# Performance work log

Hardware: AMD Instinct MI355X
Metric: run time of the kernel (lower is better)

Reference implementation:

```python
import jax, jax.numpy as jnp
import numpy as np


def _conv(x, kernel):
    # x: [N, C, H, W], kernel: [O, I, kh, kw]; torch conv2d padding=1 (symmetric both dims)
    return jax.lax.conv_general_dilated(
        x, kernel, window_strides=(1, 1), padding=((1, 1), (1, 1)),
        dimension_numbers=("NCHW", "OIHW", "NCHW"))


def setup_inputs() -> dict:
    key = jax.random.key(0)
    k1, k2 = jax.random.split(key)
    shape = (2, 7, 7, 3, 256, 256)  # bs, ah, aw, c, h, w
    infer = jax.random.normal(k1, shape, dtype=jnp.float32)
    ref = jax.random.normal(k2, shape, dtype=jnp.float32)
    return {"infer": infer, "ref": ref}


def reference(infer, ref):
    bs, ah, aw, c, h, w = infer.shape
    x = infer.reshape(bs * ah * aw, c, h, w)
    y = ref.reshape(bs * ah * aw, c, h, w)
    # fixed gradient kernels, identical across all 3x3 in/out channel pairs
    kh = jnp.broadcast_to(
        jnp.array([-0.5, 0.0, 0.5], jnp.float32).reshape(1, 1, 1, 3), (3, 3, 1, 3))
    kv = jnp.broadcast_to(
        jnp.array([-0.5, 0.0, 0.5], jnp.float32).reshape(1, 1, 3, 1), (3, 3, 3, 1))
    # torch padding=1 on a (1,3) kernel -> output (h+2, w); on (3,1) -> (h, w+2)
    loss_h = jnp.mean(jnp.abs(_conv(x, kh) - _conv(y, kh)))
    loss_v = jnp.mean(jnp.abs(_conv(x, kv) - _conv(y, kv)))
    return (loss_h + loss_v) / 2.0
```

## Files before the change

### kernel.cpp

```cpp
#include <hip/hip_runtime.h>


#define W 256
#define NIMG 98
#define CH_STRIDE 65536
#define TH 4
#define NSTRIP 64
#define NBLK (NIMG * NSTRIP)
#define SCALE (0.25f / 6472704.0f)

__device__ __forceinline__ float4 load_D_row(const float* __restrict__ xb,
                                             const float* __restrict__ yb, int r) {
  float4 d = make_float4(0.f, 0.f, 0.f, 0.f);
  if (r >= 0 && r < 256) {
    const int off = r * W;
    #pragma unroll
    for (int c = 0; c < 3; ++c) {
      float4 xv = *(const float4*)(xb + c * CH_STRIDE + off);
      float4 yv = *(const float4*)(yb + c * CH_STRIDE + off);
      d.x += xv.x - yv.x;
      d.y += xv.y - yv.y;
      d.z += xv.z - yv.z;
      d.w += xv.w - yv.w;
    }
  }
  return d;
}

__global__ __launch_bounds__(64) void detail_stage1(
    const float* __restrict__ x, const float* __restrict__ y,
    float* __restrict__ partial) {
  const int lane  = threadIdx.x;
  const int b     = blockIdx.x;
  const int n     = b >> 6;
  const int strip = b & 63;
  const int r0    = strip * TH;

  const float* xb = x + (size_t)n * 3 * CH_STRIDE + (lane << 2);
  const float* yb = y + (size_t)n * 3 * CH_STRIDE + (lane << 2);

  float4 Dm = load_D_row(xb, yb, r0 - 1);
  float4 D0 = load_D_row(xb, yb, r0);
  float acc = 0.f;

  #pragma unroll
  for (int i = 0; i < TH; ++i) {
    float4 Dp = load_D_row(xb, yb, r0 + i + 1);
    float left  = __shfl_up(D0.w, 1, 64);
    float right = __shfl_down(D0.x, 1, 64);
    if (lane == 0)  left  = 0.f;
    if (lane == 63) right = 0.f;
    acc += fabsf(D0.y - left)  + fabsf(D0.z - D0.x)
         + fabsf(D0.w - D0.y)  + fabsf(right - D0.z)
         + fabsf(Dp.x - Dm.x)  + fabsf(Dp.y - Dm.y)
         + fabsf(Dp.z - Dm.z)  + fabsf(Dp.w - Dm.w);
    Dm = D0; D0 = Dp;
  }

  #pragma unroll
  for (int off = 32; off > 0; off >>= 1)
    acc += __shfl_down(acc, off, 64);
  if (lane == 0) partial[b] = acc;
}

__global__ __launch_bounds__(64) void detail_stage1_atomic(
    const float* __restrict__ x, const float* __restrict__ y,
    float* __restrict__ out) {
  const int lane  = threadIdx.x;
  const int b     = blockIdx.x;
  const int n     = b >> 6;
  const int strip = b & 63;
  const int r0    = strip * TH;
  const float* xb = x + (size_t)n * 3 * CH_STRIDE + (lane << 2);
  const float* yb = y + (size_t)n * 3 * CH_STRIDE + (lane << 2);
  float4 Dm = load_D_row(xb, yb, r0 - 1);
  float4 D0 = load_D_row(xb, yb, r0);
  float acc = 0.f;
  #pragma unroll
  for (int i = 0; i < TH; ++i) {
    float4 Dp = load_D_row(xb, yb, r0 + i + 1);
    float left  = __shfl_up(D0.w, 1, 64);
    float right = __shfl_down(D0.x, 1, 64);
    if (lane == 0)  left  = 0.f;
    if (lane == 63) right = 0.f;
    acc += fabsf(D0.y - left)  + fabsf(D0.z - D0.x)
         + fabsf(D0.w - D0.y)  + fabsf(right - D0.z)
         + fabsf(Dp.x - Dm.x)  + fabsf(Dp.y - Dm.y)
         + fabsf(Dp.z - Dm.z)  + fabsf(Dp.w - Dm.w);
    Dm = D0; D0 = Dp;
  }
  #pragma unroll
  for (int off = 32; off > 0; off >>= 1)
    acc += __shfl_down(acc, off, 64);
  if (lane == 0) atomicAdd(out, acc * SCALE);
}

__global__ __launch_bounds__(256) void detail_stage2(
    const float* __restrict__ partial, float* __restrict__ out) {
  float acc = 0.f;
  for (int i = threadIdx.x; i < NBLK; i += 256) acc += partial[i];
  #pragma unroll
  for (int off = 32; off > 0; off >>= 1)
    acc += __shfl_down(acc, off, 64);
  __shared__ float ws[4];
  if ((threadIdx.x & 63) == 0) ws[threadIdx.x >> 6] = acc;
  __syncthreads();
  if (threadIdx.x == 0) out[0] = (ws[0] + ws[1] + ws[2] + ws[3]) * SCALE;
}

extern "C" void kernel_launch(void* const* d_in, const int* in_sizes, int n_in,
                              void* d_out, int out_size, void* d_ws, size_t ws_size,
                              hipStream_t stream) {
  const float* infer = (const float*)d_in[0];
  const float* ref   = (const float*)d_in[1];
  float* out = (float*)d_out;

  if (ws_size >= NBLK * sizeof(float)) {
    float* partial = (float*)d_ws;
    detail_stage1<<<NBLK, 64, 0, stream>>>(infer, ref, partial);
    detail_stage2<<<1, 256, 0, stream>>>(partial, out);
  } else {
    hipMemsetAsync(out, 0, sizeof(float), stream);
    detail_stage1_atomic<<<NBLK, 64, 0, stream>>>(infer, ref, out);
  }
}
```

Measured before the change: 173.5 us.

## Stage channel-summed difference rows in shared memory with 256-thread blocks

Each block now covers 8 output rows with 256 threads. Four wavefronts cooperatively load the 10 halo rows, each issuing all its loads up front, and write the channel-summed difference into a shared-memory tile. Each thread then computes the horizontal and vertical gradient terms for one column from shared memory. This lowers halo overhead from 6/4 to 10/8 rows loaded per output row and exposes more memory-level parallelism per wave. The cost is a block barrier, shared-memory traffic, and higher register pressure from holding 18 float4 loads.

```diff
diff --git a/kernel.cpp b/kernel.cpp
--- a/kernel.cpp
+++ b/kernel.cpp
@@ -4,95 +4,80 @@
 #define W 256
 #define NIMG 98
 #define CH_STRIDE 65536
-#define TH 4
-#define NSTRIP 64
+#define TH 8
+#define HALO (TH + 2)
+#define NSTRIP 32
 #define NBLK (NIMG * NSTRIP)
 #define SCALE (0.25f / 6472704.0f)
 
-__device__ __forceinline__ float4 load_D_row(const float* __restrict__ xb,
-                                             const float* __restrict__ yb, int r) {
-  float4 d = make_float4(0.f, 0.f, 0.f, 0.f);
-  if (r >= 0 && r < 256) {
-    const int off = r * W;
-    #pragma unroll
-    for (int c = 0; c < 3; ++c) {
-      float4 xv = *(const float4*)(xb + c * CH_STRIDE + off);
-      float4 yv = *(const float4*)(yb + c * CH_STRIDE + off);
-      d.x += xv.x - yv.x;
-      d.y += xv.y - yv.y;
-      d.z += xv.z - yv.z;
-      d.w += xv.w - yv.w;
-    }
-  }
-  return d;
-}
-
-__global__ __launch_bounds__(64) void detail_stage1(
+__global__ __launch_bounds__(256) void detail_stage1(
     const float* __restrict__ x, const float* __restrict__ y,
     float* __restrict__ partial) {
-  const int lane  = threadIdx.x;
+  __shared__ float D[HALO][W];
+
+  const int tid   = threadIdx.x;
+  const int lane  = tid & 63;
+  const int wv    = tid >> 6;
   const int b     = blockIdx.x;
-  const int n     = b >> 6;
-  const int strip = b & 63;
+  const int n     = b >> 5;
+  const int strip = b & 31;
   const int r0    = strip * TH;
 
   const float* xb = x + (size_t)n * 3 * CH_STRIDE + (lane << 2);
   const float* yb = y + (size_t)n * 3 * CH_STRIDE + (lane << 2);
 
-  float4 Dm = load_D_row(xb, yb, r0 - 1);
-  float4 D0 = load_D_row(xb, yb, r0);
-  float acc = 0.f;
+  const int nrows = (wv < 2) ? 3 : 2;
+  float4 vx[3][3], vy[3][3];
+  #pragma unroll
+  for (int j = 0; j < 3; ++j) {
+    if (j < nrows) {
+      const int g  = r0 - 1 + (wv + 4 * j);
+      const bool ok = (g >= 0) && (g < 256);
+      const int off = g * W;
+      #pragma unroll
+      for (int c = 0; c < 3; ++c) {
+        if (ok) {
+          vx[j][c] = *(const float4*)(xb + c * CH_STRIDE + off);
+          vy[j][c] = *(const float4*)(yb + c * CH_STRIDE + off);
+        } else {
+          vx[j][c] = make_float4(0.f, 0.f, 0.f, 0.f);
+          vy[j][c] = make_float4(0.f, 0.f, 0.f, 0.f);
+        }
+      }
+    }
+  }
 
   #pragma unroll
-  for (int i = 0; i < TH; ++i) {
-    float4 Dp = load_D_row(xb, yb, r0 + i + 1);
-    float left  = __shfl_up(D0.w, 1, 64);
-    float right = __shfl_down(D0.x, 1, 64);
-    if (lane == 0)  left  = 0.f;
-    if (lane == 63) right = 0.f;
-    acc += fabsf(D0.y - left)  + fabsf(D0.z - D0.x)
-         + fabsf(D0.w - D0.y)  + fabsf(right - D0.z)
-         + fabsf(Dp.x - Dm.x)  + fabsf(Dp.y - Dm.y)
-         + fabsf(Dp.z - Dm.z)  + fabsf(Dp.w - Dm.w);
-    Dm = D0; D0 = Dp;
+  for (int j = 0; j < 3; ++j) {
+    if (j < nrows) {
+      const int lr = wv + 4 * j;
+      float4 d;
+      d.x = (vx[j][0].x - vy[j][0].x) + (vx[j][1].x - vy[j][1].x) + (vx[j][2].x - vy[j][2].x);
+      d.y = (vx[j][0].y - vy[j][0].y) + (vx[j][1].y - vy[j][1].y) + (vx[j][2].y - vy[j][2].y);
+      d.z = (vx[j][0].z - vy[j][0].z) + (vx[j][1].z - vy[j][1].z) + (vx[j][2].z - vy[j][2].z);
+      d.w = (vx[j][0].w - vy[j][0].w) + (vx[j][1].w - vy[j][1].w) + (vx[j][2].w - vy[j][2].w);
+      *(float4*)&D[lr][lane << 2] = d;
+    }
+  }
+  __syncthreads();
+
+  const int w = tid;
+  float acc = 0.f;
+  #pragma unroll
+  for (int r = 0; r < TH; ++r) {
+    const float* rp = D[r + 1];
+    float left  = (w > 0)     ? rp[w - 1] : 0.f;
+    float right = (w < W - 1) ? rp[w + 1] : 0.f;
+    acc += fabsf(right - left) + fabsf(D[r + 2][w] - D[r][w]);
   }
 
   #pragma unroll
   for (int off = 32; off > 0; off >>= 1)
     acc += __shfl_down(acc, off, 64);
-  if (lane == 0) partial[b] = acc;
-}
-
-__global__ __launch_bounds__(64) void detail_stage1_atomic(
-    const float* __restrict__ x, const float* __restrict__ y,
-    float* __restrict__ out) {
-  const int lane  = threadIdx.x;
-  const int b     = blockIdx.x;
-  const int n     = b >> 6;
-  const int strip = b & 63;
-  const int r0    = strip * TH;
-  const float* xb = x + (size_t)n * 3 * CH_STRIDE + (lane << 2);
-  const float* yb = y + (size_t)n * 3 * CH_STRIDE + (lane << 2);
-  float4 Dm = load_D_row(xb, yb, r0 - 1);
-  float4 D0 = load_D_row(xb, yb, r0);
-  float acc = 0.f;
-  #pragma unroll
-  for (int i = 0; i < TH; ++i) {
-    float4 Dp = load_D_row(xb, yb, r0 + i + 1);
-    float left  = __shfl_up(D0.w, 1, 64);
-    float right = __shfl_down(D0.x, 1, 64);
-    if (lane == 0)  left  = 0.f;
-    if (lane == 63) right = 0.f;
-    acc += fabsf(D0.y - left)  + fabsf(D0.z - D0.x)
-         + fabsf(D0.w - D0.y)  + fabsf(right - D0.z)
-         + fabsf(Dp.x - Dm.x)  + fabsf(Dp.y - Dm.y)
-         + fabsf(Dp.z - Dm.z)  + fabsf(Dp.w - Dm.w);
-    Dm = D0; D0 = Dp;
-  }
-  #pragma unroll
-  for (int off = 32; off > 0; off >>= 1)
-    acc += __shfl_down(acc, off, 64);
-  if (lane == 0) atomicAdd(out, acc * SCALE);
+  __shared__ float ws[4];
+  if (lane == 0) ws[wv] = acc;
+  __syncthreads();
+  if (tid == 0) partial[b] = ws[0] + ws[1] + ws[2] + ws[3];
 }
 
 __global__ __launch_bounds__(256) void detail_stage2(
@@ -108,6 +93,70 @@
   if (threadIdx.x == 0) out[0] = (ws[0] + ws[1] + ws[2] + ws[3]) * SCALE;
 }
 
+__global__ __launch_bounds__(256) void detail_stage1_atomic(
+    const float* __restrict__ x, const float* __restrict__ y,
+    float* __restrict__ out) {
+  __shared__ float D[HALO][W];
+  const int tid   = threadIdx.x;
+  const int lane  = tid & 63;
+  const int wv    = tid >> 6;
+  const int b     = blockIdx.x;
+  const int n     = b >> 5;
+  const int strip = b & 31;
+  const int r0    = strip * TH;
+  const float* xb = x + (size_t)n * 3 * CH_STRIDE + (lane << 2);
+  const float* yb = y + (size_t)n * 3 * CH_STRIDE + (lane << 2);
+  const int nrows = (wv < 2) ? 3 : 2;
+  float4 vx[3][3], vy[3][3];
+  #pragma unroll
+  for (int j = 0; j < 3; ++j) {
+    if (j < nrows) {
+      const int g  = r0 - 1 + (wv + 4 * j);
+      const bool ok = (g >= 0) && (g < 256);
+      const int off = g * W;
+      #pragma unroll
+      for (int c = 0; c < 3; ++c) {
+        if (ok) {
+          vx[j][c] = *(const float4*)(xb + c * CH_STRIDE + off);
+          vy[j][c] = *(const float4*)(yb + c * CH_STRIDE + off);
+        } else {
+          vx[j][c] = make_float4(0.f, 0.f, 0.f, 0.f);
+          vy[j][c] = make_float4(0.f, 0.f, 0.f, 0.f);
+        }
+      }
+    }
+  }
+  #pragma unroll
+  for (int j = 0; j < 3; ++j) {
+    if (j < nrows) {
+      const int lr = wv + 4 * j;
+      float4 d;
+      d.x = (vx[j][0].x - vy[j][0].x) + (vx[j][1].x - vy[j][1].x) + (vx[j][2].x - vy[j][2].x);
+      d.y = (vx[j][0].y - vy[j][0].y) + (vx[j][1].y - vy[j][1].y) + (vx[j][2].y - vy[j][2].y);
+      d.z = (vx[j][0].z - vy[j][0].z) + (vx[j][1].z - vy[j][1].z) + (vx[j][2].z - vy[j][2].z);
+      d.w = (vx[j][0].w - vy[j][0].w) + (vx[j][1].w - vy[j][1].w) + (vx[j][2].w - vy[j][2].w);
+      *(float4*)&D[lr][lane << 2] = d;
+    }
+  }
+  __syncthreads();
+  const int w = tid;
+  float acc = 0.f;
+  #pragma unroll
+  for (int r = 0; r < TH; ++r) {
+    const float* rp = D[r + 1];
+    float left  = (w > 0)     ? rp[w - 1] : 0.f;
+    float right = (w < W - 1) ? rp[w + 1] : 0.f;
+    acc += fabsf(right - left) + fabsf(D[r + 2][w] - D[r][w]);
+  }
+  #pragma unroll
+  for (int off = 32; off > 0; off >>= 1)
+    acc += __shfl_down(acc, off, 64);
+  __shared__ float ws[4];
+  if (lane == 0) ws[wv] = acc;
+  __syncthreads();
+  if (tid == 0) atomicAdd(out, (ws[0] + ws[1] + ws[2] + ws[3]) * SCALE);
+}
+
 extern "C" void kernel_launch(void* const* d_in, const int* in_sizes, int n_in,
                               void* d_out, int out_size, void* d_ws, size_t ws_size,
                               hipStream_t stream) {
@@ -117,10 +166,10 @@
 
   if (ws_size >= NBLK * sizeof(float)) {
     float* partial = (float*)d_ws;
-    detail_stage1<<<NBLK, 64, 0, stream>>>(infer, ref, partial);
+    detail_stage1<<<NBLK, 256, 0, stream>>>(infer, ref, partial);
     detail_stage2<<<1, 256, 0, stream>>>(partial, out);
   } else {
     hipMemsetAsync(out, 0, sizeof(float), stream);
-    detail_stage1_atomic<<<NBLK, 64, 0, stream>>>(infer, ref, out);
+    detail_stage1_atomic<<<NBLK, 256, 0, stream>>>(infer, ref, out);
   }
 }
```

Result: no change. 172.2 us (-0.7%).
